# Kernel tuning notes

Measured on AMD Instinct MI355X. Metric: run time of the kernel, lower is better.

The kernel has to match this reference:

```python
import jax, jax.numpy as jnp
import numpy as np

B, T, E, A, S, H = 1024, 64, 1024, 10, 30, 200  # batch, time, embed, actdim, stoch, deter==hidden
MIN_STD = 0.1


def _xavier(key, fan_in, fan_out):
    lim = float(np.sqrt(6.0 / (fan_in + fan_out)))
    return jax.random.uniform(key, (fan_in, fan_out), jnp.float32, -lim, lim)


def setup_inputs() -> dict:
    key = jax.random.key(0)
    ks = jax.random.split(key, 20)
    gl = 1.0 / float(np.sqrt(H))  # torch GRUCell default init bound
    inp = {
        'embed': jax.random.normal(ks[0], (B, T, E), jnp.float32),
        'action': jax.random.normal(ks[1], (B, T, A), jnp.float32),
        'eps_post': jax.random.normal(ks[2], (T, B, S), jnp.float32),
        'eps_prior': jax.random.normal(ks[3], (T, B, S), jnp.float32),
        # Linear weights stored [in, out] (transposed vs torch) so x @ W works.
        'img1_w': _xavier(ks[4], A + S, H), 'img1_b': jnp.zeros((H,), jnp.float32),
        'gru_wi': jax.random.uniform(ks[5], (H, 3 * H), jnp.float32, -gl, gl),
        'gru_wh': jax.random.uniform(ks[6], (H, 3 * H), jnp.float32, -gl, gl),
        'gru_bi': jax.random.uniform(ks[7], (3 * H,), jnp.float32, -gl, gl),
        'gru_bh': jax.random.uniform(ks[8], (3 * H,), jnp.float32, -gl, gl),
        'img2_w': _xavier(ks[9], H, H), 'img2_b': jnp.zeros((H,), jnp.float32),
        'img3_w': _xavier(ks[10], H, 2 * S), 'img3_b': jnp.zeros((2 * S,), jnp.float32),
        'obs1_w': _xavier(ks[11], H + E, H), 'obs1_b': jnp.zeros((H,), jnp.float32),
        'obs2_w': _xavier(ks[12], H, 2 * S), 'obs2_b': jnp.zeros((2 * S,), jnp.float32),
    }
    return inp


def _observe(embed, action, eps_post, eps_prior,
             img1_w, img1_b, gru_wi, gru_wh, gru_bi, gru_bh,
             img2_w, img2_b, img3_w, img3_b, obs1_w, obs1_b, obs2_w, obs2_b):
    elu = jax.nn.elu
    embed_t = jnp.transpose(embed, (1, 0, 2))   # [T,B,E]
    action_t = jnp.transpose(action, (1, 0, 2))  # [T,B,A]

    def step(carry, xs):
        stoch, deter = carry
        a, emb, ep_q, ep_p = xs
        # img_step (prior)
        x = elu(jnp.concatenate([stoch, a], -1) @ img1_w + img1_b)
        gi = x @ gru_wi + gru_bi
        gh = deter @ gru_wh + gru_bh
        ir, iz, i_n = jnp.split(gi, 3, axis=-1)
        hr, hz, h_n = jnp.split(gh, 3, axis=-1)
        r = jax.nn.sigmoid(ir + hr)
        z = jax.nn.sigmoid(iz + hz)
        n = jnp.tanh(i_n + r * h_n)
        deter = (1.0 - z) * n + z * deter
        y = elu(deter @ img2_w + img2_b) @ img3_w + img3_b
        p_mean, p_std = jnp.split(y, 2, axis=-1)
        p_std = jax.nn.softplus(p_std) + MIN_STD
        p_stoch = p_mean + p_std * ep_p  # rsample
        # obs_step (posterior)
        o = elu(jnp.concatenate([deter, emb], -1) @ obs1_w + obs1_b) @ obs2_w + obs2_b
        q_mean, q_std = jnp.split(o, 2, axis=-1)
        q_std = jax.nn.softplus(q_std) + MIN_STD
        q_stoch = q_mean + q_std * ep_q  # rsample
        out = jnp.concatenate([q_mean, q_std, q_stoch, deter,
                               p_mean, p_std, p_stoch, deter], axis=-1)
        return (q_stoch, deter), out

    init = (jnp.zeros((B, S), embed.dtype), jnp.zeros((B, H), embed.dtype))
    _, outs = jax.lax.scan(step, init, (action_t, embed_t, eps_post, eps_prior))
    # outs: [T, B, 2*(3S+H)] -> [B, T, 580]; layout: post(mean,std,stoch,deter)|prior(mean,std,stoch,deter)
    return jnp.transpose(outs, (1, 0, 2))


def reference(embed, action, eps_post, eps_prior,
              img1_w, img1_b, gru_wi, gru_wh, gru_bi, gru_bh,
              img2_w, img2_b, img3_w, img3_b, obs1_w, obs1_b, obs2_w, obs2_b):
    return _observe(embed, action, eps_post, eps_prior,
                    img1_w, img1_b, gru_wi, gru_wh, gru_bi, gru_bh,
                    img2_w, img2_b, img3_w, img3_b, obs1_w, obs1_b, obs2_w, obs2_b)
```

## Files before the change

### kernel.cpp

```cpp
#include <hip/hip_runtime.h>

#define T_ 64

typedef __attribute__((ext_vector_type(4))) float f32x4;
typedef __attribute__((ext_vector_type(8))) short s16x8;

__device__ __forceinline__ unsigned short f2bf(float f) {
  unsigned u = __float_as_uint(f);
  u = (u + 0x7FFFu + ((u >> 16) & 1u)) >> 16;
  return (unsigned short)u;
}
__device__ __forceinline__ float bf2f(unsigned short h) {
  return __uint_as_float(((unsigned)h) << 16);
}
__device__ __forceinline__ float eluf(float x) { return x > 0.f ? x : __expf(x) - 1.f; }
__device__ __forceinline__ float sigmf(float x) { return 1.f / (1.f + __expf(-x)); }
__device__ __forceinline__ float tanh_(float x) {
  float xx = fminf(fmaxf(x, -30.f), 30.f);
  float e = __expf(-2.f * xx);
  return (1.f - e) / (1.f + e);
}
__device__ __forceinline__ float softpf(float x) {
  return x > 20.f ? x : __logf(1.f + __expf(x));
}

#define OPW1   0
#define OPWI   6656
#define OPWH   126464
#define OPO1D  246272
#define OPO2   286208
#define OPI2   298496
#define OPI3   345088
#define OWIWT  359424
#define OWHWT  364416
#define OO1DWT 369408
#define OI1WT  371072
#define OO2WT  372736
#define PK_U16 373248

#define OFF_PK  26214400
#define OFF_SWZ 26960896

__device__ void pack_mat(int idx, int stride, const float* __restrict__ W,
                         int K, int N, int KT, int NT, unsigned short* __restrict__ dst) {
  int total = KT * NT * 512;
  for (int i = idx; i < total; i += stride) {
    int j = i & 7, l = (i >> 3) & 63, rem = i >> 9;
    int kt = rem % KT, nt = rem / KT;
    int n = nt * 16 + (l & 15), k = kt * 32 + (l >> 4) * 8 + j;
    float v = (k < K && n < N) ? W[(size_t)k * N + n] : 0.f;
    dst[i] = f2bf(v);
  }
}

__device__ void pack_gate(int idx, int stride, const float* __restrict__ W,
                          unsigned short* __restrict__ dst) {
  int total = 3 * 13 * 6 * 512;
  for (int i = idx; i < total; i += stride) {
    int j = i & 7, l = (i >> 3) & 63, rem = i >> 9;
    int kt = rem % 6, rem2 = rem / 6, nt = rem2 % 13, g = rem2 / 13;
    int u = nt * 16 + (l & 15);
    int k = kt * 32 + (l >> 4) * 8 + j;
    float v = (u < 200) ? W[(size_t)k * 600 + g * 200 + u] : 0.f;
    dst[i] = f2bf(v);
  }
}

__global__ void prep_weights(const float* __restrict__ w1, const float* __restrict__ wi,
                             const float* __restrict__ wh, const float* __restrict__ i2,
                             const float* __restrict__ i3, const float* __restrict__ obs1w,
                             const float* __restrict__ o2,
                             unsigned short* __restrict__ pk,
                             unsigned short* __restrict__ swz) {
  int idx = blockIdx.x * blockDim.x + threadIdx.x;
  int stride = gridDim.x * blockDim.x;
  pack_mat(idx, stride, w1, 40, 200, 1, 13, pk + OPW1);
  pack_gate(idx, stride, wi, pk + OPWI);
  pack_gate(idx, stride, wh, pk + OPWH);
  pack_mat(idx, stride, obs1w, 200, 200, 6, 13, pk + OPO1D);
  pack_mat(idx, stride, o2, 200, 60, 6, 4, pk + OPO2);
  pack_mat(idx, stride, i2, 200, 200, 7, 13, pk + OPI2);
  pack_mat(idx, stride, i3, 200, 60, 7, 4, pk + OPI3);
  for (int i = idx; i < 4992; i += stride) {
    int j = i & 7, c = (i >> 3) % 208, g = i / 1664;
    pk[OWIWT + i] = f2bf((c < 200) ? wi[(size_t)(192 + j) * 600 + g * 200 + c] : 0.f);
    pk[OWHWT + i] = f2bf((c < 200) ? wh[(size_t)(192 + j) * 600 + g * 200 + c] : 0.f);
  }
  for (int i = idx; i < 1664; i += stride) {
    int c = i >> 3, j = i & 7;
    pk[OO1DWT + i] = f2bf((c < 200) ? obs1w[(size_t)(192 + j) * 200 + c] : 0.f);
    pk[OI1WT + i]  = f2bf((c < 200) ? w1[(size_t)(32 + j) * 200 + c] : 0.f);
  }
  for (int i = idx; i < 512; i += stride) {
    int c = i >> 3, j = i & 7;
    pk[OO2WT + i] = f2bf((c < 60) ? o2[(size_t)(192 + j) * 60 + c] : 0.f);
  }
  for (int i = idx; i < 212992; i += stride) {
    int j = i & 7, l = (i >> 3) & 63, rem = i >> 9;
    int nt = rem % 13, kc = rem / 13;
    int k = kc * 32 + ((l >> 4) * 8) + j;
    int n = nt * 16 + (l & 15);
    float v = (n < 200) ? obs1w[(size_t)(200 + k) * 200 + n] : 0.0f;
    swz[i] = f2bf(v);
  }
}

__global__ __launch_bounds__(256) void emb_gemm(const float* __restrict__ embed,
                                                const float* __restrict__ obs1b,
                                                const unsigned short* __restrict__ swz,
                                                unsigned short* __restrict__ emb_pre) {
  __shared__ __align__(16) unsigned short lds_A[64][40];
  int tid = threadIdx.x;
  int lane = tid & 63, w = tid >> 6;
  int R0 = blockIdx.x * 64;
  int tt = R0 >> 10;
  int bb = R0 & 1023;

  f32x4 acc[13];
#pragma unroll
  for (int nt = 0; nt < 13; ++nt) acc[nt] = (f32x4){0.f, 0.f, 0.f, 0.f};

  int i_row = tid >> 2, cg = tid & 3;
  const float* arow = embed + ((size_t)(bb + i_row) * 64 + tt) * 1024 + cg * 8;

  for (int kc = 0; kc < 32; ++kc) {
    __syncthreads();
    {
      const float* p = arow + kc * 32;
      f32x4 a0 = *(const f32x4*)p;
      f32x4 a1 = *(const f32x4*)(p + 4);
      unsigned short* dst = &lds_A[i_row][cg * 8];
      dst[0] = f2bf(a0[0]); dst[1] = f2bf(a0[1]); dst[2] = f2bf(a0[2]); dst[3] = f2bf(a0[3]);
      dst[4] = f2bf(a1[0]); dst[5] = f2bf(a1[1]); dst[6] = f2bf(a1[2]); dst[7] = f2bf(a1[3]);
    }
    __syncthreads();
    s16x8 af = *(const s16x8*)&lds_A[w * 16 + (lane & 15)][(lane >> 4) * 8];
    const unsigned short* bp = swz + (size_t)kc * 6656 + (size_t)lane * 8;
#pragma unroll
    for (int nt = 0; nt < 13; ++nt) {
      s16x8 bfv = *(const s16x8*)(bp + nt * 512);
      acc[nt] = __builtin_amdgcn_mfma_f32_16x16x32_bf16(af, bfv, acc[nt], 0, 0, 0);
    }
  }
  int r0 = R0 + w * 16 + ((lane >> 4) << 2);
  int c0 = lane & 15;
#pragma unroll
  for (int nt = 0; nt < 13; ++nt) {
    int n = nt * 16 + c0;
    if (n < 200) {
      float bv = obs1b[n];
#pragma unroll
      for (int rr = 0; rr < 4; ++rr)
        emb_pre[(size_t)(r0 + rr) * 200 + n] = f2bf(acc[nt][rr] + bv);
    }
  }
}

#define WAITVC(n) asm volatile("s_waitcnt vmcnt(" #n ")" ::: "memory")
#define LGKM0  asm volatile("s_waitcnt lgkmcnt(0)" ::: "memory")
#define MEMCLB asm volatile("" ::: "memory")
#define BAR()  __builtin_amdgcn_s_barrier()
#define SCHED0 __builtin_amdgcn_sched_barrier(0)
#define MFMA16(A, B, C) __builtin_amdgcn_mfma_f32_16x16x32_bf16((A), (B), (C), 0, 0, 0)

typedef __attribute__((address_space(3))) unsigned int u32_lds;
typedef const __attribute__((address_space(1))) unsigned int u32_glb;

__device__ __forceinline__ void gll16(const unsigned short* g, unsigned short* l, int lane) {
  __builtin_amdgcn_global_load_lds((u32_glb*)(g + lane * 8), (u32_lds*)l, 16, 0, 0);
}

__global__ __launch_bounds__(256, 1) void scan_v6(
    const float* __restrict__ action, const float* __restrict__ eps_post,
    const float* __restrict__ img1_b, const float* __restrict__ gru_bi,
    const float* __restrict__ gru_bh, const float* __restrict__ obs2_b,
    const unsigned short* __restrict__ pk, const unsigned short* __restrict__ emb_pre,
    float* __restrict__ out) {

  __shared__ __align__(16) unsigned short ring[4][12][512];
  __shared__ __align__(16) unsigned short l_w1[13 * 512];
  __shared__ __align__(16) unsigned short l_o2[24 * 512];
  __shared__ __align__(16) unsigned short l_wiWT[3][208][8];
  __shared__ __align__(16) unsigned short l_whWT[3][208][8];
  __shared__ __align__(16) unsigned short l_o1dWT[208][8];
  __shared__ __align__(16) unsigned short l_i1WT[208][8];
  __shared__ __align__(16) unsigned short l_o2WT[64][8];
  __shared__ __align__(16) unsigned short zblk[8];
  __shared__ __align__(16) unsigned short xoA[28][16][8];
  __shared__ __align__(16) unsigned short dA[28][16][8];
  __shared__ __align__(16) unsigned short sA[8][16][8];
  __shared__ __align__(16) float s_o[60][20];
  __shared__ __align__(16) float outbuf[16][292];
  __shared__ unsigned l_toff[4][96];

  const int tid = threadIdx.x, lane = tid & 63, w = tid >> 6;
  const int arow = lane & 15, kg = lane >> 4;
  const int b0 = blockIdx.x * 16;
  const int nug = (w == 0) ? 4 : 3;
  const int SW = nug * 24;
  unsigned short* ringw = &ring[w][0][0];

  for (int i = tid; i < 28 * 16 * 8; i += 256) { (&xoA[0][0][0])[i] = 0; (&dA[0][0][0])[i] = 0; }
  for (int i = tid; i < 8 * 16 * 8; i += 256) (&sA[0][0][0])[i] = 0;
  for (int i = tid; i < 13 * 512; i += 256) l_w1[i] = pk[OPW1 + i];
  for (int i = tid; i < 24 * 512; i += 256) l_o2[i] = pk[OPO2 + i];
  for (int i = tid; i < 4992; i += 256) (&l_wiWT[0][0][0])[i] = pk[OWIWT + i];
  for (int i = tid; i < 4992; i += 256) (&l_whWT[0][0][0])[i] = pk[OWHWT + i];
  for (int i = tid; i < 1664; i += 256) (&l_o1dWT[0][0])[i] = pk[OO1DWT + i];
  for (int i = tid; i < 1664; i += 256) (&l_i1WT[0][0])[i] = pk[OI1WT + i];
  for (int i = tid; i < 512; i += 256) (&l_o2WT[0][0])[i] = pk[OO2WT + i];
  if (tid < 8) zblk[tid] = 0;
  for (int i = tid; i < 4 * 96; i += 256) {
    int ww = i / 96, tau = i % 96;
    int iu = tau / 24, r2 = tau % 24, q = r2 / 6, kt = r2 % 6;
    int ug = ww + 4 * iu;
    unsigned off;
    if (q < 3) off = OPWI + (unsigned)((q * 13 + (ug <= 12 ? ug : 12)) * 6 + kt) * 512;
    else       off = OPWH + (unsigned)((2 * 13 + (ug <= 12 ? ug : 12)) * 6 + kt) * 512;
    l_toff[ww][tau] = off;
  }

  s16x8 wB[10][6];
#pragma unroll
  for (int s = 0; s < 10; ++s) {
    const unsigned short* base;
    if (w == 0) {
      if (s < 8) { int iu = s >> 1, g = s & 1; base = pk + OPWH + (size_t)((g * 13 + 4 * iu) * 6) * 512; }
      else if (s == 8) base = pk + OPO1D + (size_t)(12 * 6) * 512;
      else base = pk + OPO1D;
    } else {
      if (s < 6) { int iu = s >> 1, g = s & 1; base = pk + OPWH + (size_t)((g * 13 + (w + 4 * iu)) * 6) * 512; }
      else base = pk + OPO1D + (size_t)(((w - 1) + 3 * (s - 6)) * 6) * 512;
    }
#pragma unroll
    for (int kt = 0; kt < 6; ++kt)
      wB[s][kt] = *(const s16x8*)(base + (size_t)kt * 512 + lane * 8);
  }

  float bsum[4][2], bi2[4], bh2[4];
#pragma unroll
  for (int iu = 0; iu < 4; ++iu) {
    int u = (w + 4 * iu) * 16 + arow;
    bool vld = (iu < nug) && (u < 200);
    int uc = vld ? u : 0;
    float m = vld ? 1.f : 0.f;
    bsum[iu][0] = m * (gru_bi[uc] + gru_bh[uc]);
    bsum[iu][1] = m * (gru_bi[200 + uc] + gru_bh[200 + uc]);
    bi2[iu] = m * gru_bi[400 + uc];
    bh2[iu] = m * gru_bh[400 + uc];
  }
  float b1v[4];
#pragma unroll
  for (int i = 0; i < 4; ++i) {
    int nt = (i < 3) ? (w + 4 * i) : 12;
    int c = nt * 16 + arow;
    b1v[i] = (c < 200) ? img1_b[c] : 0.f;
  }
  float b5 = ((w * 16 + arow) < 60) ? obs2_b[w * 16 + arow] : 0.f;

  unsigned short e16[16];
#pragma unroll
  for (int i = 0; i < 4; ++i) {
    int nt4 = (w == 0) ? 12 : ((w - 1) + 3 * i);
    int c = nt4 * 16 + arow; int cc = (c < 200) ? c : 199;
#pragma unroll
    for (int rr = 0; rr < 4; ++rr)
      e16[i * 4 + rr] = emb_pre[((size_t)(b0 + kg * 4 + rr)) * 200 + cc];
  }
  float epsv[2];
  { int i1 = (tid + 256 < 480) ? tid + 256 : 479;
    epsv[0] = eps_post[((size_t)(b0 + tid / 30)) * 30 + tid % 30];
    epsv[1] = eps_post[((size_t)(b0 + i1 / 30)) * 30 + i1 % 30]; }
  float act0, actn;
  { int sl = (lane < 40) ? (w * 40 + lane) : (w * 40);
    act0 = action[((size_t)(b0 + sl / 10) * T_ + 0) * 10 + sl % 10];
    actn = action[((size_t)(b0 + sl / 10) * T_ + 1) * 10 + sl % 10]; }
  f32x4 dv[4];
#pragma unroll
  for (int iu = 0; iu < 4; ++iu) dv[iu] = (f32x4){0.f, 0.f, 0.f, 0.f};

  __syncthreads();
  if (lane < 40) {
    int sl = w * 40 + lane; int kk = sl % 10, r = sl / 10;
    sA[(30 + kk) >> 3][r][(30 + kk) & 7] = f2bf(act0);
  }
#pragma unroll
  for (int tt = 0; tt < 12; ++tt)
    gll16(pk + l_toff[w][tt], ringw + tt * 512, lane);
  WAITVC(0);
  __syncthreads();

  for (int t = 0; t < T_; ++t) {
    {
      s16x8 a0 = *(const s16x8*)&sA[kg][arow][0];
      s16x8 a1 = *(const s16x8*)&sA[4 + kg][arow][0];
#pragma unroll
      for (int i = 0; i < 4; ++i) {
        if (i < 3 || w == 0) {
          int nt = (i < 3) ? (w + 4 * i) : 12;
          int c = nt * 16 + arow;
          s16x8 B0 = *(const s16x8*)&l_w1[nt * 512 + lane * 8];
          f32x4 acc = {b1v[i], b1v[i], b1v[i], b1v[i]};
          acc = MFMA16(a0, B0, acc);
          s16x8 B1 = *(const s16x8*)((kg == 0) ? &l_i1WT[c][0] : &zblk[0]);
          acc = MFMA16(a1, B1, acc);
          if (c < 200) {
#pragma unroll
            for (int rr = 0; rr < 4; ++rr)
              xoA[c >> 3][kg * 4 + rr][c & 7] = f2bf(eluf(acc[rr]));
          }
        }
      }
    }
    LGKM0; BAR();

    {
#pragma unroll
      for (int iu = 0; iu < 4; ++iu) {
        if (iu < 3 || w == 0) {
          const int uu = (w + 4 * iu) * 16 + arow;
          const int uuc = (uu < 208) ? uu : 207;
          s16x8 ax[6], ad[6];
#pragma unroll
          for (int kt = 0; kt < 6; ++kt) {
            ax[kt] = *(const s16x8*)&xoA[kt * 4 + kg][arow][0];
            ad[kt] = *(const s16x8*)&dA[kt * 4 + kg][arow][0];
          }
          s16x8 ax6 = *(const s16x8*)&xoA[24 + kg][arow][0];
          s16x8 ad6 = *(const s16x8*)&dA[24 + kg][arow][0];
          f32x4 gv[2], gin, ghn;
#pragma unroll
          for (int q = 0; q < 4; ++q) {
            const int beta = iu * 4 + q;
            if (beta < 2) { WAITVC(30); } else { WAITVC(6); }
            float b = (q < 2) ? bsum[iu][q & 1] : ((q == 2) ? bi2[iu] : bh2[iu]);
            f32x4 acc = {b, b, b, b};
#pragma unroll
            for (int kt = 0; kt < 6; ++kt) {
              const int slot = (beta * 6 + kt) % 12;
              s16x8 Bv = *(const s16x8*)(ringw + slot * 512 + lane * 8);
              acc = MFMA16((q == 3) ? ad[kt] : ax[kt], Bv, acc);
            }
            MEMCLB; SCHED0;
#pragma unroll
            for (int k2 = 0; k2 < 6; ++k2) {
              const int ttc = beta * 6 + 12 + k2;
              int tm = (ttc >= SW) ? ttc - SW : ttc;
              gll16(pk + l_toff[w][tm], ringw + ((ttc % 12) * 512), lane);
            }
            if (q < 2) {
              { const unsigned short* wp = (kg == 0) ? &l_wiWT[q][uuc][0] : &zblk[0];
                acc = MFMA16(ax6, *(const s16x8*)wp, acc); }
              const int s_ = iu * 2 + q;
#pragma unroll
              for (int kt = 0; kt < 6; ++kt) acc = MFMA16(ad[kt], wB[s_][kt], acc);
              { const unsigned short* wp = (kg == 0) ? &l_whWT[q][uuc][0] : &zblk[0];
                acc = MFMA16(ad6, *(const s16x8*)wp, acc); }
              gv[q] = acc;
            } else if (q == 2) {
              const unsigned short* wp = (kg == 0) ? &l_wiWT[2][uuc][0] : &zblk[0];
              gin = MFMA16(ax6, *(const s16x8*)wp, acc);
            } else {
              const unsigned short* wp = (kg == 0) ? &l_whWT[2][uuc][0] : &zblk[0];
              ghn = MFMA16(ad6, *(const s16x8*)wp, acc);
            }
          }
#pragma unroll
          for (int rr = 0; rr < 4; ++rr) {
            float r = sigmf(gv[0][rr]);
            float z = sigmf(gv[1][rr]);
            float n = tanh_(gin[rr] + r * ghn[rr]);
            dv[iu][rr] = (1.f - z) * n + z * dv[iu][rr];
          }
          if (uu < 200) {
#pragma unroll
            for (int rr = 0; rr < 4; ++rr) outbuf[kg * 4 + rr][90 + uu] = dv[iu][rr];
          }
        }
      }
    }
    LGKM0; BAR();

#pragma unroll
    for (int iu = 0; iu < 4; ++iu) {
      if (iu < 3 || w == 0) {
        int uu = (w + 4 * iu) * 16 + arow;
        if (uu < 200) {
#pragma unroll
          for (int rr = 0; rr < 4; ++rr)
            dA[uu >> 3][kg * 4 + rr][uu & 7] = f2bf(dv[iu][rr]);
        }
      }
    }
    LGKM0; BAR();

    {
      s16x8 ad4[6];
#pragma unroll
      for (int kt = 0; kt < 6; ++kt) ad4[kt] = *(const s16x8*)&dA[kt * 4 + kg][arow][0];
      s16x8 ad46 = *(const s16x8*)&dA[24 + kg][arow][0];
      if (w == 0) {
        int c = 192 + arow;
        f32x4 acc = {0.f, 0.f, 0.f, 0.f};
#pragma unroll
        for (int kt = 0; kt < 6; ++kt) acc = MFMA16(ad4[kt], wB[8][kt], acc);
        { const unsigned short* wp = (kg == 0) ? &l_o1dWT[c][0] : &zblk[0];
          acc = MFMA16(ad46, *(const s16x8*)wp, acc); }
        if (c < 200) {
#pragma unroll
          for (int rr = 0; rr < 4; ++rr)
            xoA[c >> 3][kg * 4 + rr][c & 7] = f2bf(eluf(acc[rr] + bf2f(e16[rr])));
        }
      } else {
#pragma unroll
        for (int i = 0; i < 4; ++i) {
          int c = ((w - 1) + 3 * i) * 16 + arow;
          f32x4 acc = {0.f, 0.f, 0.f, 0.f};
#pragma unroll
          for (int kt = 0; kt < 6; ++kt) acc = MFMA16(ad4[kt], wB[6 + i][kt], acc);
          { const unsigned short* wp = (kg == 0) ? &l_o1dWT[c][0] : &zblk[0];
            acc = MFMA16(ad46, *(const s16x8*)wp, acc); }
#pragma unroll
          for (int rr = 0; rr < 4; ++rr)
            xoA[c >> 3][kg * 4 + rr][c & 7] = f2bf(eluf(acc[rr] + bf2f(e16[i * 4 + rr])));
        }
      }
    }
    LGKM0; BAR();

    {
      s16x8 a5[6];
#pragma unroll
      for (int kt = 0; kt < 6; ++kt) a5[kt] = *(const s16x8*)&xoA[kt * 4 + kg][arow][0];
      s16x8 a56 = *(const s16x8*)&xoA[24 + kg][arow][0];
      int c5 = w * 16 + arow;
      f32x4 acc = {b5, b5, b5, b5};
#pragma unroll
      for (int kt = 0; kt < 6; ++kt) {
        s16x8 Bv = *(const s16x8*)&l_o2[(w * 6 + kt) * 512 + lane * 8];
        acc = MFMA16(a5[kt], Bv, acc);
      }
      { const unsigned short* wp = (kg == 0) ? &l_o2WT[c5][0] : &zblk[0];
        acc = MFMA16(a56, *(const s16x8*)wp, acc); }
      if (c5 < 60) *(f32x4*)&s_o[c5][kg * 4] = acc;
    }
    LGKM0; BAR();

    {
#pragma unroll
      for (int rep = 0; rep < 2; ++rep) {
        int it = tid + rep * 256;
        bool v = it < 480;
        int itc = v ? it : 479;
        int r = itc / 30, j = itc % 30;
        float qm = s_o[j][r];
        float qs = softpf(s_o[j + 30][r]) + 0.1f;
        float qst = qm + qs * epsv[rep];
        if (v) {
          outbuf[r][j] = qm; outbuf[r][30 + j] = qs; outbuf[r][60 + j] = qst;
          sA[j >> 3][r][j & 7] = f2bf(qst);
        }
      }
      if (lane < 40) {
        int sl = w * 40 + lane; int kk = sl % 10, r = sl / 10;
        sA[(30 + kk) >> 3][r][(30 + kk) & 7] = f2bf(actn);
      }
      int tc = (t + 1 < T_) ? t + 1 : T_ - 1;
      int ta = (t + 2 < T_) ? t + 2 : T_ - 1;
#pragma unroll
      for (int i = 0; i < 4; ++i) {
        int nt4 = (w == 0) ? 12 : ((w - 1) + 3 * i);
        int c = nt4 * 16 + arow; int cc = (c < 200) ? c : 199;
#pragma unroll
        for (int rr = 0; rr < 4; ++rr)
          e16[i * 4 + rr] = emb_pre[((size_t)tc * 1024 + b0 + kg * 4 + rr) * 200 + cc];
      }
      { int i1 = (tid + 256 < 480) ? tid + 256 : 479;
        epsv[0] = eps_post[((size_t)tc * 1024 + b0 + tid / 30) * 30 + tid % 30];
        epsv[1] = eps_post[((size_t)tc * 1024 + b0 + i1 / 30) * 30 + i1 % 30]; }
      { int sl = (lane < 40) ? (w * 40 + lane) : (w * 40);
        actn = action[((size_t)(b0 + sl / 10) * T_ + ta) * 10 + sl % 10]; }
    }
    LGKM0; BAR();

#pragma unroll
    for (int k2 = 0; k2 < 5; ++k2) {
      int idx = tid + k2 * 256; idx = (idx < 1168) ? idx : 1167;
      int row = idx / 73, ci = idx - row * 73;
      f32x4 v = *(const f32x4*)&outbuf[row][ci * 4];
      *(f32x4*)(out + ((size_t)(b0 + row) * T_ + t) * 580 + ci * 4) = v;
    }
  }
}

__global__ __launch_bounds__(256) void post_head(const float* __restrict__ eps_prior,
                                                 const float* __restrict__ img2_b,
                                                 const float* __restrict__ img3_b,
                                                 const unsigned short* __restrict__ pk,
                                                 float* __restrict__ out) {
  __shared__ __align__(16) unsigned short dAp[4][28][16][8];
  __shared__ __align__(16) unsigned short y1p[4][28][16][8];
  __shared__ __align__(16) float s_p[60][68];
  int b = blockIdx.x;
  int tid = threadIdx.x;
  int lane = tid & 63, w = tid >> 6, arow = lane & 15, kg = lane >> 4;

  for (int i = tid; i < 1536; i += 256) {
    int mt = i / 384, rem = i % 384;
    int gidx = 25 + rem / 128, r2 = (rem % 128) / 8, j = rem & 7;
    dAp[mt][gidx][r2][j] = 0;
    y1p[mt][gidx][r2][j] = 0;
  }
  for (int i = tid; i < 12800; i += 256) {
    int row = i / 200, c = i % 200;
    float v = out[((size_t)(b * 64 + row)) * 580 + 90 + c];
    dAp[row >> 4][c >> 3][row & 15][c & 7] = f2bf(v);
  }
  __syncthreads();

  s16x8 ad[7];
#pragma unroll
  for (int kt = 0; kt < 7; ++kt) ad[kt] = *(const s16x8*)&dAp[w][kt * 4 + kg][arow][0];
#pragma unroll
  for (int nt = 0; nt < 13; ++nt) {
    int col = nt * 16 + arow;
    float bv = (col < 200) ? img2_b[col] : 0.f;
    f32x4 acc = {bv, bv, bv, bv};
#pragma unroll
    for (int kt = 0; kt < 7; ++kt) {
      s16x8 Bv = *(const s16x8*)(pk + OPI2 + (size_t)((nt * 7 + kt) * 512) + lane * 8);
      acc = __builtin_amdgcn_mfma_f32_16x16x32_bf16(ad[kt], Bv, acc, 0, 0, 0);
    }
    if (col < 200) {
#pragma unroll
      for (int rr = 0; rr < 4; ++rr)
        y1p[w][col >> 3][kg * 4 + rr][col & 7] = f2bf(eluf(acc[rr]));
    }
  }
  __syncthreads();

  s16x8 ay[7];
#pragma unroll
  for (int kt = 0; kt < 7; ++kt) ay[kt] = *(const s16x8*)&y1p[w][kt * 4 + kg][arow][0];
#pragma unroll
  for (int nt = 0; nt < 4; ++nt) {
    int col = nt * 16 + arow;
    float bv = (col < 60) ? img3_b[col] : 0.f;
    f32x4 acc = {bv, bv, bv, bv};
#pragma unroll
    for (int kt = 0; kt < 7; ++kt) {
      s16x8 Bv = *(const s16x8*)(pk + OPI3 + (size_t)((nt * 7 + kt) * 512) + lane * 8);
      acc = __builtin_amdgcn_mfma_f32_16x16x32_bf16(ay[kt], Bv, acc, 0, 0, 0);
    }
    if (col < 60) {
#pragma unroll
      for (int rr = 0; rr < 4; ++rr) s_p[col][w * 16 + kg * 4 + rr] = acc[rr];
    }
  }
  __syncthreads();

  for (int i = tid; i < 1920; i += 256) {
    int row = i / 30, j = i % 30;
    float pm = s_p[j][row];
    float ps = softpf(s_p[j + 30][row]) + 0.1f;
    float pst = pm + ps * eps_prior[((size_t)row * 1024 + b) * 30 + j];
    size_t ob = ((size_t)b * 64 + row) * 580;
    out[ob + 290 + j] = pm;
    out[ob + 320 + j] = ps;
    out[ob + 350 + j] = pst;
  }
  for (int i = tid; i < 6400; i += 256) {
    int row = i / 100, c2 = i % 100;
    size_t ob = ((size_t)b * 64 + row) * 580;
    *(float2*)&out[ob + 380 + c2 * 2] = *(const float2*)&out[ob + 90 + c2 * 2];
  }
}

extern "C" void kernel_launch(void* const* d_in, const int* in_sizes, int n_in,
                              void* d_out, int out_size, void* d_ws, size_t ws_size,
                              hipStream_t stream) {
  const float* embed    = (const float*)d_in[0];
  const float* action   = (const float*)d_in[1];
  const float* eps_post = (const float*)d_in[2];
  const float* eps_prior= (const float*)d_in[3];
  const float* img1_w   = (const float*)d_in[4];
  const float* img1_b   = (const float*)d_in[5];
  const float* gru_wi   = (const float*)d_in[6];
  const float* gru_wh   = (const float*)d_in[7];
  const float* gru_bi   = (const float*)d_in[8];
  const float* gru_bh   = (const float*)d_in[9];
  const float* img2_w   = (const float*)d_in[10];
  const float* img2_b   = (const float*)d_in[11];
  const float* img3_w   = (const float*)d_in[12];
  const float* img3_b   = (const float*)d_in[13];
  const float* obs1_w   = (const float*)d_in[14];
  const float* obs1_b   = (const float*)d_in[15];
  const float* obs2_w   = (const float*)d_in[16];
  const float* obs2_b   = (const float*)d_in[17];

  char* ws = (char*)d_ws;
  unsigned short* emb_pre = (unsigned short*)ws;
  unsigned short* pkw     = (unsigned short*)(ws + OFF_PK);
  unsigned short* swz     = (unsigned short*)(ws + OFF_SWZ);
  float* outp = (float*)d_out;

  prep_weights<<<256, 256, 0, stream>>>(img1_w, gru_wi, gru_wh, img2_w, img3_w,
                                        obs1_w, obs2_w, pkw, swz);
  emb_gemm<<<1024, 256, 0, stream>>>(embed, obs1_b, swz, emb_pre);
  scan_v6<<<64, 256, 0, stream>>>(action, eps_post, img1_b, gru_bi, gru_bh,
                                  obs2_b, pkw, emb_pre, outp);
  post_head<<<1024, 256, 0, stream>>>(eps_prior, img2_b, img3_b, pkw, outp);
}
```

Baseline: 996.2 us.

## Double scan block to 8 waves and redistribute GRU/obs tiles with streamed weight ring

```diff
diff --git a/kernel.cpp b/kernel.cpp
--- a/kernel.cpp
+++ b/kernel.cpp
@@ -156,12 +156,14 @@
   }
 }
 
-#define WAITVC(n) asm volatile("s_waitcnt vmcnt(" #n ")" ::: "memory")
 #define LGKM0  asm volatile("s_waitcnt lgkmcnt(0)" ::: "memory")
 #define MEMCLB asm volatile("" ::: "memory")
 #define BAR()  __builtin_amdgcn_s_barrier()
-#define SCHED0 __builtin_amdgcn_sched_barrier(0)
 #define MFMA16(A, B, C) __builtin_amdgcn_mfma_f32_16x16x32_bf16((A), (B), (C), 0, 0, 0)
+#define WV9  asm volatile("s_waitcnt vmcnt(9)" ::: "memory")
+#define WV29 asm volatile("s_waitcnt vmcnt(29)" ::: "memory")
+#define WV4  asm volatile("s_waitcnt vmcnt(4)" ::: "memory")
+#define WV0  asm volatile("s_waitcnt vmcnt(0)" ::: "memory")
 
 typedef __attribute__((address_space(3))) unsigned int u32_lds;
 typedef const __attribute__((address_space(1))) unsigned int u32_glb;
@@ -170,16 +172,62 @@
   __builtin_amdgcn_global_load_lds((u32_glb*)(g + lane * 8), (u32_lds*)l, 16, 0, 0);
 }
 
-__global__ __launch_bounds__(256, 1) void scan_v6(
+template <int TB, bool BIGB>
+__device__ __forceinline__ f32x4 cons6(const s16x8* A, f32x4 acc,
+                                       unsigned short* ringw, const unsigned* toffw,
+                                       const unsigned short* pk, int lane) {
+#pragma unroll
+  for (int kt = 0; kt < 6; ++kt) {
+    const int tau = TB + kt;
+    if ((tau & 3) == 0) {
+      if (tau < 8) { if (BIGB) { WV29; } else { WV9; } }
+      else { WV4; }
+    }
+    s16x8 Bv = *(const s16x8*)(ringw + (tau & 7) * 512 + lane * 8);
+    acc = MFMA16(A[kt], Bv, acc);
+    if ((tau & 3) == 3) {
+      LGKM0; MEMCLB;
+#pragma unroll
+      for (int k2 = 1; k2 <= 4; ++k2) {
+        const int tile = (tau + 4 + k2) % 48;
+        gll16(pk + toffw[tile], ringw + (tile & 7) * 512, lane);
+      }
+      MEMCLB;
+    }
+  }
+  return acc;
+}
+
+__device__ __forceinline__ f32x4 res6(const s16x8* A, const s16x8* Wt, f32x4 acc) {
+#pragma unroll
+  for (int kt = 0; kt < 6; ++kt) acc = MFMA16(A[kt], Wt[kt], acc);
+  return acc;
+}
+__device__ __forceinline__ f32x4 rem1(const s16x8& A6, const unsigned short* wt,
+                                      const unsigned short* zb, bool kg0, f32x4 acc) {
+  const unsigned short* p = kg0 ? wt : zb;
+  return MFMA16(A6, *(const s16x8*)p, acc);
+}
+__device__ __forceinline__ void grustep(const f32x4& rv, const f32x4& zv,
+                                        const f32x4& inv, const f32x4& hnv, f32x4& dv) {
+#pragma unroll
+  for (int rr = 0; rr < 4; ++rr) {
+    float r = sigmf(rv[rr]);
+    float z = sigmf(zv[rr]);
+    float n = tanh_(inv[rr] + r * hnv[rr]);
+    dv[rr] = (1.f - z) * n + z * dv[rr];
+  }
+}
+
+__global__ __launch_bounds__(512, 1) void scan_v7(
     const float* __restrict__ action, const float* __restrict__ eps_post,
     const float* __restrict__ img1_b, const float* __restrict__ gru_bi,
     const float* __restrict__ gru_bh, const float* __restrict__ obs2_b,
     const unsigned short* __restrict__ pk, const unsigned short* __restrict__ emb_pre,
     float* __restrict__ out) {
 
-  __shared__ __align__(16) unsigned short ring[4][12][512];
+  __shared__ __align__(16) unsigned short ring[8][8][512];
   __shared__ __align__(16) unsigned short l_w1[13 * 512];
-  __shared__ __align__(16) unsigned short l_o2[24 * 512];
   __shared__ __align__(16) unsigned short l_wiWT[3][208][8];
   __shared__ __align__(16) unsigned short l_whWT[3][208][8];
   __shared__ __align__(16) unsigned short l_o1dWT[208][8];
@@ -191,305 +239,345 @@
   __shared__ __align__(16) unsigned short sA[8][16][8];
   __shared__ __align__(16) float s_o[60][20];
   __shared__ __align__(16) float outbuf[16][292];
-  __shared__ unsigned l_toff[4][96];
+  __shared__ unsigned l_toff[8][48];
 
   const int tid = threadIdx.x, lane = tid & 63, w = tid >> 6;
   const int arow = lane & 15, kg = lane >> 4;
+  const bool kg0 = (kg == 0);
   const int b0 = blockIdx.x * 16;
-  const int nug = (w == 0) ? 4 : 3;
-  const int SW = nug * 24;
   unsigned short* ringw = &ring[w][0][0];
-
-  for (int i = tid; i < 28 * 16 * 8; i += 256) { (&xoA[0][0][0])[i] = 0; (&dA[0][0][0])[i] = 0; }
-  for (int i = tid; i < 8 * 16 * 8; i += 256) (&sA[0][0][0])[i] = 0;
-  for (int i = tid; i < 13 * 512; i += 256) l_w1[i] = pk[OPW1 + i];
-  for (int i = tid; i < 24 * 512; i += 256) l_o2[i] = pk[OPO2 + i];
-  for (int i = tid; i < 4992; i += 256) (&l_wiWT[0][0][0])[i] = pk[OWIWT + i];
-  for (int i = tid; i < 4992; i += 256) (&l_whWT[0][0][0])[i] = pk[OWHWT + i];
-  for (int i = tid; i < 1664; i += 256) (&l_o1dWT[0][0])[i] = pk[OO1DWT + i];
-  for (int i = tid; i < 1664; i += 256) (&l_i1WT[0][0])[i] = pk[OI1WT + i];
-  for (int i = tid; i < 512; i += 256) (&l_o2WT[0][0])[i] = pk[OO2WT + i];
+  const unsigned* toffw = &l_toff[w][0];
+
+  for (int i = tid; i < 28 * 16 * 8; i += 512) { (&xoA[0][0][0])[i] = 0; (&dA[0][0][0])[i] = 0; }
+  for (int i = tid; i < 8 * 16 * 8; i += 512) (&sA[0][0][0])[i] = 0;
+  for (int i = tid; i < 13 * 512; i += 512) l_w1[i] = pk[OPW1 + i];
+  for (int i = tid; i < 4992; i += 512) {
+    (&l_wiWT[0][0][0])[i] = pk[OWIWT + i];
+    (&l_whWT[0][0][0])[i] = pk[OWHWT + i];
+  }
+  for (int i = tid; i < 1664; i += 512) {
+    (&l_o1dWT[0][0])[i] = pk[OO1DWT + i];
+    (&l_i1WT[0][0])[i] = pk[OI1WT + i];
+  }
+  for (int i = tid; i < 512; i += 512) (&l_o2WT[0][0])[i] = pk[OO2WT + i];
   if (tid < 8) zblk[tid] = 0;
-  for (int i = tid; i < 4 * 96; i += 256) {
-    int ww = i / 96, tau = i % 96;
-    int iu = tau / 24, r2 = tau % 24, q = r2 / 6, kt = r2 % 6;
-    int ug = ww + 4 * iu;
+  for (int i = tid; i < 8 * 48; i += 512) {
+    int ww = i / 48, tau = i % 48;
     unsigned off;
-    if (q < 3) off = OPWI + (unsigned)((q * 13 + (ug <= 12 ? ug : 12)) * 6 + kt) * 512;
-    else       off = OPWH + (unsigned)((2 * 13 + (ug <= 12 ? ug : 12)) * 6 + kt) * 512;
+    if (ww < 5) {
+      if (tau < 18) { int g = tau / 6, kt = tau % 6; off = OPWI + ((g * 13 + ww) * 6 + kt) * 512; }
+      else {
+        int t2 = tau - 18, ug = ww + 8;
+        if (t2 < 6)       off = OPWI + ((0 * 13 + ug) * 6 + t2) * 512;
+        else if (t2 < 12) off = OPWI + ((1 * 13 + ug) * 6 + (t2 - 6)) * 512;
+        else if (t2 < 18) off = OPWH + ((1 * 13 + ug) * 6 + (t2 - 12)) * 512;
+        else if (t2 < 24) off = OPWI + ((2 * 13 + ug) * 6 + (t2 - 18)) * 512;
+        else              off = OPWH + ((2 * 13 + ug) * 6 + (t2 - 24)) * 512;
+      }
+    } else {
+      if (tau < 18) { int g = tau / 6, kt = tau % 6; off = OPWI + ((g * 13 + ww) * 6 + kt) * 512; }
+      else if (tau < 42) {
+        int i4 = (tau - 18) / 6, kt = (tau - 18) % 6;
+        int nt = (ww - 5) * 4 + i4;
+        off = OPO1D + (nt * 6 + kt) * 512;
+      } else {
+        int kt = tau - 42;
+        int nt5 = (ww == 5) ? 0 : (ww == 6) ? 1 : 3;
+        off = OPO2 + (nt5 * 6 + kt) * 512;
+      }
+    }
     l_toff[ww][tau] = off;
   }
 
-  s16x8 wB[10][6];
-#pragma unroll
-  for (int s = 0; s < 10; ++s) {
-    const unsigned short* base;
-    if (w == 0) {
-      if (s < 8) { int iu = s >> 1, g = s & 1; base = pk + OPWH + (size_t)((g * 13 + 4 * iu) * 6) * 512; }
-      else if (s == 8) base = pk + OPO1D + (size_t)(12 * 6) * 512;
-      else base = pk + OPO1D;
+  s16x8 wB[4][6];
+  {
+    const unsigned short* base[4];
+    if (w < 5) {
+      base[0] = pk + OPWH + (size_t)((0 * 13 + w) * 6) * 512;
+      base[1] = pk + OPWH + (size_t)((1 * 13 + w) * 6) * 512;
+      base[2] = pk + OPWH + (size_t)((2 * 13 + w) * 6) * 512;
+      base[3] = pk + OPWH + (size_t)((0 * 13 + w + 8) * 6) * 512;
     } else {
-      if (s < 6) { int iu = s >> 1, g = s & 1; base = pk + OPWH + (size_t)((g * 13 + (w + 4 * iu)) * 6) * 512; }
-      else base = pk + OPO1D + (size_t)(((w - 1) + 3 * (s - 6)) * 6) * 512;
-    }
-#pragma unroll
-    for (int kt = 0; kt < 6; ++kt)
-      wB[s][kt] = *(const s16x8*)(base + (size_t)kt * 512 + lane * 8);
-  }
-
-  float bsum[4][2], bi2[4], bh2[4];
-#pragma unroll
-  for (int iu = 0; iu < 4; ++iu) {
-    int u = (w + 4 * iu) * 16 + arow;
-    bool vld = (iu < nug) && (u < 200);
-    int uc = vld ? u : 0;
-    float m = vld ? 1.f : 0.f;
-    bsum[iu][0] = m * (gru_bi[uc] + gru_bh[uc]);
-    bsum[iu][1] = m * (gru_bi[200 + uc] + gru_bh[200 + uc]);
-    bi2[iu] = m * gru_bi[400 + uc];
-    bh2[iu] = m * gru_bh[400 + uc];
-  }
-  float b1v[4];
-#pragma unroll
-  for (int i = 0; i < 4; ++i) {
-    int nt = (i < 3) ? (w + 4 * i) : 12;
-    int c = nt * 16 + arow;
-    b1v[i] = (c < 200) ? img1_b[c] : 0.f;
-  }
-  float b5 = ((w * 16 + arow) < 60) ? obs2_b[w * 16 + arow] : 0.f;
-
-  unsigned short e16[16];
-#pragma unroll
-  for (int i = 0; i < 4; ++i) {
-    int nt4 = (w == 0) ? 12 : ((w - 1) + 3 * i);
-    int c = nt4 * 16 + arow; int cc = (c < 200) ? c : 199;
-#pragma unroll
-    for (int rr = 0; rr < 4; ++rr)
-      e16[i * 4 + rr] = emb_pre[((size_t)(b0 + kg * 4 + rr)) * 200 + cc];
-  }
-  float epsv[2];
-  { int i1 = (tid + 256 < 480) ? tid + 256 : 479;
-    epsv[0] = eps_post[((size_t)(b0 + tid / 30)) * 30 + tid % 30];
-    epsv[1] = eps_post[((size_t)(b0 + i1 / 30)) * 30 + i1 % 30]; }
+      base[0] = pk + OPWH + (size_t)((0 * 13 + w) * 6) * 512;
+      base[1] = pk + OPWH + (size_t)((1 * 13 + w) * 6) * 512;
+      base[2] = pk + OPWH + (size_t)((2 * 13 + w) * 6) * 512;
+      if (w == 5)      base[3] = pk + OPO1D + (size_t)(12 * 6) * 512;
+      else if (w == 7) base[3] = pk + OPO2 + (size_t)(2 * 6) * 512;
+      else             base[3] = pk + OPO1D;
+    }
+#pragma unroll
+    for (int s = 0; s < 4; ++s)
+#pragma unroll
+      for (int kt = 0; kt < 6; ++kt)
+        wB[s][kt] = *(const s16x8*)(base[s] + (size_t)kt * 512 + lane * 8);
+  }
+
+  const int uA = w * 16 + arow;
+  const int uB = (w + 8) * 16 + arow;
+  const bool mB = (w < 5) && (uB < 200);
+  const int uBc = (uB < 200) ? uB : 199;
+  float bsA0 = gru_bi[uA] + gru_bh[uA];
+  float bsA1 = gru_bi[200 + uA] + gru_bh[200 + uA];
+  float bi2a = gru_bi[400 + uA], bh2a = gru_bh[400 + uA];
+  float bsB0 = mB ? (gru_bi[uBc] + gru_bh[uBc]) : 0.f;
+  float bsB1 = mB ? (gru_bi[200 + uBc] + gru_bh[200 + uBc]) : 0.f;
+  float bi2b = mB ? gru_bi[400 + uBc] : 0.f;
+  float bh2b = mB ? gru_bh[400 + uBc] : 0.f;
+  float b1A = img1_b[uA];
+  float b1B = mB ? img1_b[uBc] : 0.f;
+  float b5a = 0.f, b5b = 0.f;
+  if (w == 5) b5a = obs2_b[arow];
+  else if (w == 6) b5a = obs2_b[16 + arow];
+  else if (w == 7) { b5a = (48 + arow < 60) ? obs2_b[48 + arow] : 0.f; b5b = obs2_b[32 + arow]; }
+
+  unsigned short e16[20];
+#pragma unroll
+  for (int i = 0; i < 20; ++i) e16[i] = 0;
+  if (w >= 5) {
+#pragma unroll
+    for (int i = 0; i < 5; ++i) {
+      int nt = (w == 5) ? ((i < 4) ? i : 12) : ((w == 6) ? (4 + ((i < 4) ? i : 3)) : (8 + ((i < 4) ? i : 3)));
+      int c = nt * 16 + arow; int cc = (c < 200) ? c : 199;
+#pragma unroll
+      for (int rr = 0; rr < 4; ++rr)
+        e16[i * 4 + rr] = emb_pre[((size_t)(b0 + kg * 4 + rr)) * 200 + cc];
+    }
+  }
+  float epsv;
+  { int it = (tid < 480) ? tid : 479;
+    epsv = eps_post[((size_t)(b0 + it / 30)) * 30 + it % 30]; }
   float act0, actn;
-  { int sl = (lane < 40) ? (w * 40 + lane) : (w * 40);
+  { int sl = (lane < 20) ? (w * 20 + lane) : (w * 20);
     act0 = action[((size_t)(b0 + sl / 10) * T_ + 0) * 10 + sl % 10];
     actn = action[((size_t)(b0 + sl / 10) * T_ + 1) * 10 + sl % 10]; }
-  f32x4 dv[4];
-#pragma unroll
-  for (int iu = 0; iu < 4; ++iu) dv[iu] = (f32x4){0.f, 0.f, 0.f, 0.f};
+  f32x4 dv0 = {0.f, 0.f, 0.f, 0.f}, dv1 = {0.f, 0.f, 0.f, 0.f};
 
   __syncthreads();
-  if (lane < 40) {
-    int sl = w * 40 + lane; int kk = sl % 10, r = sl / 10;
+  if (lane < 20) {
+    int sl = w * 20 + lane; int kk = sl % 10, r = sl / 10;
     sA[(30 + kk) >> 3][r][(30 + kk) & 7] = f2bf(act0);
   }
 #pragma unroll
-  for (int tt = 0; tt < 12; ++tt)
-    gll16(pk + l_toff[w][tt], ringw + tt * 512, lane);
-  WAITVC(0);
+  for (int tt = 0; tt < 8; ++tt) gll16(pk + toffw[tt], ringw + tt * 512, lane);
+  WV0;
   __syncthreads();
 
   for (int t = 0; t < T_; ++t) {
     {
       s16x8 a0 = *(const s16x8*)&sA[kg][arow][0];
       s16x8 a1 = *(const s16x8*)&sA[4 + kg][arow][0];
-#pragma unroll
-      for (int i = 0; i < 4; ++i) {
-        if (i < 3 || w == 0) {
-          int nt = (i < 3) ? (w + 4 * i) : 12;
-          int c = nt * 16 + arow;
-          s16x8 B0 = *(const s16x8*)&l_w1[nt * 512 + lane * 8];
-          f32x4 acc = {b1v[i], b1v[i], b1v[i], b1v[i]};
-          acc = MFMA16(a0, B0, acc);
-          s16x8 B1 = *(const s16x8*)((kg == 0) ? &l_i1WT[c][0] : &zblk[0]);
-          acc = MFMA16(a1, B1, acc);
-          if (c < 200) {
-#pragma unroll
-            for (int rr = 0; rr < 4; ++rr)
-              xoA[c >> 3][kg * 4 + rr][c & 7] = f2bf(eluf(acc[rr]));
-          }
+      {
+        s16x8 B0 = *(const s16x8*)&l_w1[w * 512 + lane * 8];
+        f32x4 acc = {b1A, b1A, b1A, b1A};
+        acc = MFMA16(a0, B0, acc);
+        acc = rem1(a1, &l_i1WT[uA][0], zblk, kg0, acc);
+#pragma unroll
+        for (int rr = 0; rr < 4; ++rr)
+          xoA[uA >> 3][kg * 4 + rr][uA & 7] = f2bf(eluf(acc[rr]));
+      }
+      if (w < 5) {
+        s16x8 B0 = *(const s16x8*)&l_w1[(w + 8) * 512 + lane * 8];
+        f32x4 acc = {b1B, b1B, b1B, b1B};
+        acc = MFMA16(a0, B0, acc);
+        acc = rem1(a1, &l_i1WT[uB][0], zblk, kg0, acc);
+        if (uB < 200) {
+#pragma unroll
+          for (int rr = 0; rr < 4; ++rr)
+            xoA[uB >> 3][kg * 4 + rr][uB & 7] = f2bf(eluf(acc[rr]));
         }
       }
     }
     LGKM0; BAR();
 
     {
-#pragma unroll
-      for (int iu = 0; iu < 4; ++iu) {
-        if (iu < 3 || w == 0) {
-          const int uu = (w + 4 * iu) * 16 + arow;
-          const int uuc = (uu < 208) ? uu : 207;
-          s16x8 ax[6], ad[6];
-#pragma unroll
-          for (int kt = 0; kt < 6; ++kt) {
-            ax[kt] = *(const s16x8*)&xoA[kt * 4 + kg][arow][0];
-            ad[kt] = *(const s16x8*)&dA[kt * 4 + kg][arow][0];
-          }
-          s16x8 ax6 = *(const s16x8*)&xoA[24 + kg][arow][0];
-          s16x8 ad6 = *(const s16x8*)&dA[24 + kg][arow][0];
-          f32x4 gv[2], gin, ghn;
-#pragma unroll
-          for (int q = 0; q < 4; ++q) {
-            const int beta = iu * 4 + q;
-            if (beta < 2) { WAITVC(30); } else { WAITVC(6); }
-            float b = (q < 2) ? bsum[iu][q & 1] : ((q == 2) ? bi2[iu] : bh2[iu]);
-            f32x4 acc = {b, b, b, b};
-#pragma unroll
-            for (int kt = 0; kt < 6; ++kt) {
-              const int slot = (beta * 6 + kt) % 12;
-              s16x8 Bv = *(const s16x8*)(ringw + slot * 512 + lane * 8);
-              acc = MFMA16((q == 3) ? ad[kt] : ax[kt], Bv, acc);
-            }
-            MEMCLB; SCHED0;
-#pragma unroll
-            for (int k2 = 0; k2 < 6; ++k2) {
-              const int ttc = beta * 6 + 12 + k2;
-              int tm = (ttc >= SW) ? ttc - SW : ttc;
-              gll16(pk + l_toff[w][tm], ringw + ((ttc % 12) * 512), lane);
-            }
-            if (q < 2) {
-              { const unsigned short* wp = (kg == 0) ? &l_wiWT[q][uuc][0] : &zblk[0];
-                acc = MFMA16(ax6, *(const s16x8*)wp, acc); }
-              const int s_ = iu * 2 + q;
-#pragma unroll
-              for (int kt = 0; kt < 6; ++kt) acc = MFMA16(ad[kt], wB[s_][kt], acc);
-              { const unsigned short* wp = (kg == 0) ? &l_whWT[q][uuc][0] : &zblk[0];
-                acc = MFMA16(ad6, *(const s16x8*)wp, acc); }
-              gv[q] = acc;
-            } else if (q == 2) {
-              const unsigned short* wp = (kg == 0) ? &l_wiWT[2][uuc][0] : &zblk[0];
-              gin = MFMA16(ax6, *(const s16x8*)wp, acc);
-            } else {
-              const unsigned short* wp = (kg == 0) ? &l_whWT[2][uuc][0] : &zblk[0];
-              ghn = MFMA16(ad6, *(const s16x8*)wp, acc);
-            }
-          }
-#pragma unroll
-          for (int rr = 0; rr < 4; ++rr) {
-            float r = sigmf(gv[0][rr]);
-            float z = sigmf(gv[1][rr]);
-            float n = tanh_(gin[rr] + r * ghn[rr]);
-            dv[iu][rr] = (1.f - z) * n + z * dv[iu][rr];
-          }
-          if (uu < 200) {
-#pragma unroll
-            for (int rr = 0; rr < 4; ++rr) outbuf[kg * 4 + rr][90 + uu] = dv[iu][rr];
-          }
+      s16x8 ax[6], ad[6];
+#pragma unroll
+      for (int kt = 0; kt < 6; ++kt) {
+        ax[kt] = *(const s16x8*)&xoA[kt * 4 + kg][arow][0];
+        ad[kt] = *(const s16x8*)&dA[kt * 4 + kg][arow][0];
+      }
+      s16x8 ax6 = *(const s16x8*)&xoA[24 + kg][arow][0];
+      s16x8 ad6 = *(const s16x8*)&dA[24 + kg][arow][0];
+      if (w < 5) {
+        f32x4 rv = cons6<0, false>(ax, (f32x4){bsA0, bsA0, bsA0, bsA0}, ringw, toffw, pk, lane);
+        rv = rem1(ax6, &l_wiWT[0][uA][0], zblk, kg0, rv);
+        rv = res6(ad, wB[0], rv);
+        rv = rem1(ad6, &l_whWT[0][uA][0], zblk, kg0, rv);
+        f32x4 zv = cons6<6, false>(ax, (f32x4){bsA1, bsA1, bsA1, bsA1}, ringw, toffw, pk, lane);
+        zv = rem1(ax6, &l_wiWT[1][uA][0], zblk, kg0, zv);
+        zv = res6(ad, wB[1], zv);
+        zv = rem1(ad6, &l_whWT[1][uA][0], zblk, kg0, zv);
+        f32x4 inv = cons6<12, false>(ax, (f32x4){bi2a, bi2a, bi2a, bi2a}, ringw, toffw, pk, lane);
+        inv = rem1(ax6, &l_wiWT[2][uA][0], zblk, kg0, inv);
+        f32x4 hnv = res6(ad, wB[2], (f32x4){bh2a, bh2a, bh2a, bh2a});
+        hnv = rem1(ad6, &l_whWT[2][uA][0], zblk, kg0, hnv);
+        grustep(rv, zv, inv, hnv, dv0);
+#pragma unroll
+        for (int rr = 0; rr < 4; ++rr) outbuf[kg * 4 + rr][90 + uA] = dv0[rr];
+        f32x4 rv2 = cons6<18, false>(ax, (f32x4){bsB0, bsB0, bsB0, bsB0}, ringw, toffw, pk, lane);
+        rv2 = rem1(ax6, &l_wiWT[0][uB][0], zblk, kg0, rv2);
+        rv2 = res6(ad, wB[3], rv2);
+        rv2 = rem1(ad6, &l_whWT[0][uB][0], zblk, kg0, rv2);
+        f32x4 zv2 = cons6<24, false>(ax, (f32x4){bsB1, bsB1, bsB1, bsB1}, ringw, toffw, pk, lane);
+        zv2 = cons6<30, false>(ad, zv2, ringw, toffw, pk, lane);
+        zv2 = rem1(ax6, &l_wiWT[1][uB][0], zblk, kg0, zv2);
+        zv2 = rem1(ad6, &l_whWT[1][uB][0], zblk, kg0, zv2);
+        f32x4 inv2 = cons6<36, false>(ax, (f32x4){bi2b, bi2b, bi2b, bi2b}, ringw, toffw, pk, lane);
+        inv2 = rem1(ax6, &l_wiWT[2][uB][0], zblk, kg0, inv2);
+        f32x4 hnv2 = cons6<42, false>(ad, (f32x4){bh2b, bh2b, bh2b, bh2b}, ringw, toffw, pk, lane);
+        hnv2 = rem1(ad6, &l_whWT[2][uB][0], zblk, kg0, hnv2);
+        grustep(rv2, zv2, inv2, hnv2, dv1);
+        if (uB < 200) {
+#pragma unroll
+          for (int rr = 0; rr < 4; ++rr) outbuf[kg * 4 + rr][90 + uB] = dv1[rr];
         }
+      } else {
+        f32x4 rv = cons6<0, true>(ax, (f32x4){bsA0, bsA0, bsA0, bsA0}, ringw, toffw, pk, lane);
+        rv = rem1(ax6, &l_wiWT[0][uA][0], zblk, kg0, rv);
+        rv = res6(ad, wB[0], rv);
+        rv = rem1(ad6, &l_whWT[0][uA][0], zblk, kg0, rv);
+        f32x4 zv = cons6<6, true>(ax, (f32x4){bsA1, bsA1, bsA1, bsA1}, ringw, toffw, pk, lane);
+        zv = rem1(ax6, &l_wiWT[1][uA][0], zblk, kg0, zv);
+        zv = res6(ad, wB[1], zv);
+        zv = rem1(ad6, &l_whWT[1][uA][0], zblk, kg0, zv);
+        f32x4 inv = cons6<12, true>(ax, (f32x4){bi2a, bi2a, bi2a, bi2a}, ringw, toffw, pk, lane);
+        inv = rem1(ax6, &l_wiWT[2][uA][0], zblk, kg0, inv);
+        f32x4 hnv = res6(ad, wB[2], (f32x4){bh2a, bh2a, bh2a, bh2a});
+        hnv = rem1(ad6, &l_whWT[2][uA][0], zblk, kg0, hnv);
+        grustep(rv, zv, inv, hnv, dv0);
+#pragma unroll
+        for (int rr = 0; rr < 4; ++rr) outbuf[kg * 4 + rr][90 + uA] = dv0[rr];
       }
     }
     LGKM0; BAR();
 
-#pragma unroll
-    for (int iu = 0; iu < 4; ++iu) {
-      if (iu < 3 || w == 0) {
-        int uu = (w + 4 * iu) * 16 + arow;
-        if (uu < 200) {
-#pragma unroll
-          for (int rr = 0; rr < 4; ++rr)
-            dA[uu >> 3][kg * 4 + rr][uu & 7] = f2bf(dv[iu][rr]);
-        }
+    {
+#pragma unroll
+      for (int rr = 0; rr < 4; ++rr)
+        dA[uA >> 3][kg * 4 + rr][uA & 7] = f2bf(dv0[rr]);
+      if (mB) {
+#pragma unroll
+        for (int rr = 0; rr < 4; ++rr)
+          dA[uB >> 3][kg * 4 + rr][uB & 7] = f2bf(dv1[rr]);
       }
     }
     LGKM0; BAR();
 
-    {
+    if (w >= 5) {
       s16x8 ad4[6];
 #pragma unroll
       for (int kt = 0; kt < 6; ++kt) ad4[kt] = *(const s16x8*)&dA[kt * 4 + kg][arow][0];
       s16x8 ad46 = *(const s16x8*)&dA[24 + kg][arow][0];
-      if (w == 0) {
+      const int ntb = (w - 5) * 4;
+      {
+        int c = (ntb + 0) * 16 + arow;
+        f32x4 acc = cons6<18, true>(ad4, (f32x4){0.f, 0.f, 0.f, 0.f}, ringw, toffw, pk, lane);
+        acc = rem1(ad46, &l_o1dWT[c][0], zblk, kg0, acc);
+#pragma unroll
+        for (int rr = 0; rr < 4; ++rr)
+          xoA[c >> 3][kg * 4 + rr][c & 7] = f2bf(eluf(acc[rr] + bf2f(e16[0 * 4 + rr])));
+      }
+      {
+        int c = (ntb + 1) * 16 + arow;
+        f32x4 acc = cons6<24, true>(ad4, (f32x4){0.f, 0.f, 0.f, 0.f}, ringw, toffw, pk, lane);
+        acc = rem1(ad46, &l_o1dWT[c][0], zblk, kg0, acc);
+#pragma unroll
+        for (int rr = 0; rr < 4; ++rr)
+          xoA[c >> 3][kg * 4 + rr][c & 7] = f2bf(eluf(acc[rr] + bf2f(e16[1 * 4 + rr])));
+      }
+      {
+        int c = (ntb + 2) * 16 + arow;
+        f32x4 acc = cons6<30, true>(ad4, (f32x4){0.f, 0.f, 0.f, 0.f}, ringw, toffw, pk, lane);
+        acc = rem1(ad46, &l_o1dWT[c][0], zblk, kg0, acc);
+#pragma unroll
+        for (int rr = 0; rr < 4; ++rr)
+          xoA[c >> 3][kg * 4 + rr][c & 7] = f2bf(eluf(acc[rr] + bf2f(e16[2 * 4 + rr])));
+      }
+      {
+        int c = (ntb + 3) * 16 + arow;
+        f32x4 acc = cons6<36, true>(ad4, (f32x4){0.f, 0.f, 0.f, 0.f}, ringw, toffw, pk, lane);
+        acc = rem1(ad46, &l_o1dWT[c][0], zblk, kg0, acc);
+#pragma unroll
+        for (int rr = 0; rr < 4; ++rr)
+          xoA[c >> 3][kg * 4 + rr][c & 7] = f2bf(eluf(acc[rr] + bf2f(e16[3 * 4 + rr])));
+      }
+      if (w == 5) {
         int c = 192 + arow;
-        f32x4 acc = {0.f, 0.f, 0.f, 0.f};
-#pragma unroll
-        for (int kt = 0; kt < 6; ++kt) acc = MFMA16(ad4[kt], wB[8][kt], acc);
-        { const unsigned short* wp = (kg == 0) ? &l_o1dWT[c][0] : &zblk[0];
-          acc = MFMA16(ad46, *(const s16x8*)wp, acc); }
+        f32x4 acc = res6(ad4, wB[3], (f32x4){0.f, 0.f, 0.f, 0.f});
+        acc = rem1(ad46, &l_o1dWT[c][0], zblk, kg0, acc);
         if (c < 200) {
 #pragma unroll
           for (int rr = 0; rr < 4; ++rr)
-            xoA[c >> 3][kg * 4 + rr][c & 7] = f2bf(eluf(acc[rr] + bf2f(e16[rr])));
+            xoA[c >> 3][kg * 4 + rr][c & 7] = f2bf(eluf(acc[rr] + bf2f(e16[16 + rr])));
         }
-      } else {
-#pragma unroll
-        for (int i = 0; i < 4; ++i) {
-          int c = ((w - 1) + 3 * i) * 16 + arow;
-          f32x4 acc = {0.f, 0.f, 0.f, 0.f};
-#pragma unroll
-          for (int kt = 0; kt < 6; ++kt) acc = MFMA16(ad4[kt], wB[6 + i][kt], acc);
-          { const unsigned short* wp = (kg == 0) ? &l_o1dWT[c][0] : &zblk[0];
-            acc = MFMA16(ad46, *(const s16x8*)wp, acc); }
-#pragma unroll
-          for (int rr = 0; rr < 4; ++rr)
-            xoA[c >> 3][kg * 4 + rr][c & 7] = f2bf(eluf(acc[rr] + bf2f(e16[i * 4 + rr])));
-        }
       }
     }
     LGKM0; BAR();
 
-    {
+    if (w >= 5) {
       s16x8 a5[6];
 #pragma unroll
       for (int kt = 0; kt < 6; ++kt) a5[kt] = *(const s16x8*)&xoA[kt * 4 + kg][arow][0];
       s16x8 a56 = *(const s16x8*)&xoA[24 + kg][arow][0];
-      int c5 = w * 16 + arow;
-      f32x4 acc = {b5, b5, b5, b5};
-#pragma unroll
-      for (int kt = 0; kt < 6; ++kt) {
-        s16x8 Bv = *(const s16x8*)&l_o2[(w * 6 + kt) * 512 + lane * 8];
-        acc = MFMA16(a5[kt], Bv, acc);
-      }
-      { const unsigned short* wp = (kg == 0) ? &l_o2WT[c5][0] : &zblk[0];
-        acc = MFMA16(a56, *(const s16x8*)wp, acc); }
+      int c5 = (w == 5) ? arow : (w == 6) ? (16 + arow) : (48 + arow);
+      f32x4 acc = cons6<42, true>(a5, (f32x4){b5a, b5a, b5a, b5a}, ringw, toffw, pk, lane);
+      {
+        int c5c = (c5 < 64) ? c5 : 63;
+        acc = rem1(a56, &l_o2WT[c5c][0], zblk, kg0, acc);
+      }
       if (c5 < 60) *(f32x4*)&s_o[c5][kg * 4] = acc;
+      if (w == 7) {
+        int c5r = 32 + arow;
+        f32x4 acc2 = res6(a5, wB[3], (f32x4){b5b, b5b, b5b, b5b});
+        acc2 = rem1(a56, &l_o2WT[c5r][0], zblk, kg0, acc2);
+        *(f32x4*)&s_o[c5r][kg * 4] = acc2;
+      }
     }
     LGKM0; BAR();
 
+    MEMCLB;
     {
-#pragma unroll
-      for (int rep = 0; rep < 2; ++rep) {
-        int it = tid + rep * 256;
-        bool v = it < 480;
-        int itc = v ? it : 479;
-        int r = itc / 30, j = itc % 30;
+      if (tid < 480) {
+        int r = tid / 30, j = tid % 30;
         float qm = s_o[j][r];
         float qs = softpf(s_o[j + 30][r]) + 0.1f;
-        float qst = qm + qs * epsv[rep];
-        if (v) {
-          outbuf[r][j] = qm; outbuf[r][30 + j] = qs; outbuf[r][60 + j] = qst;
-          sA[j >> 3][r][j & 7] = f2bf(qst);
-        }
-      }
-      if (lane < 40) {
-        int sl = w * 40 + lane; int kk = sl % 10, r = sl / 10;
+        float qst = qm + qs * epsv;
+        outbuf[r][j] = qm; outbuf[r][30 + j] = qs; outbuf[r][60 + j] = qst;
+        sA[j >> 3][r][j & 7] = f2bf(qst);
+      }
+      if (lane < 20) {
+        int sl = w * 20 + lane; int kk = sl % 10, r = sl / 10;
         sA[(30 + kk) >> 3][r][(30 + kk) & 7] = f2bf(actn);
       }
       int tc = (t + 1 < T_) ? t + 1 : T_ - 1;
       int ta = (t + 2 < T_) ? t + 2 : T_ - 1;
-#pragma unroll
-      for (int i = 0; i < 4; ++i) {
-        int nt4 = (w == 0) ? 12 : ((w - 1) + 3 * i);
-        int c = nt4 * 16 + arow; int cc = (c < 200) ? c : 199;
-#pragma unroll
-        for (int rr = 0; rr < 4; ++rr)
-          e16[i * 4 + rr] = emb_pre[((size_t)tc * 1024 + b0 + kg * 4 + rr) * 200 + cc];
-      }
-      { int i1 = (tid + 256 < 480) ? tid + 256 : 479;
-        epsv[0] = eps_post[((size_t)tc * 1024 + b0 + tid / 30) * 30 + tid % 30];
-        epsv[1] = eps_post[((size_t)tc * 1024 + b0 + i1 / 30) * 30 + i1 % 30]; }
-      { int sl = (lane < 40) ? (w * 40 + lane) : (w * 40);
+      MEMCLB;
+      if (w >= 5) {
+#pragma unroll
+        for (int i = 0; i < 5; ++i) {
+          int nt = (w == 5) ? ((i < 4) ? i : 12) : ((w == 6) ? (4 + ((i < 4) ? i : 3)) : (8 + ((i < 4) ? i : 3)));
+          int c = nt * 16 + arow; int cc = (c < 200) ? c : 199;
+#pragma unroll
+          for (int rr = 0; rr < 4; ++rr)
+            e16[i * 4 + rr] = emb_pre[((size_t)tc * 1024 + b0 + kg * 4 + rr) * 200 + cc];
+        }
+      }
+      { int it = (tid < 480) ? tid : 479;
+        epsv = eps_post[((size_t)tc * 1024 + b0 + it / 30) * 30 + it % 30]; }
+      { int sl = (lane < 20) ? (w * 20 + lane) : (w * 20);
         actn = action[((size_t)(b0 + sl / 10) * T_ + ta) * 10 + sl % 10]; }
+      MEMCLB;
     }
     LGKM0; BAR();
 
 #pragma unroll
-    for (int k2 = 0; k2 < 5; ++k2) {
-      int idx = tid + k2 * 256; idx = (idx < 1168) ? idx : 1167;
+    for (int k2 = 0; k2 < 3; ++k2) {
+      int idx = tid + k2 * 512; idx = (idx < 1168) ? idx : 1167;
       int row = idx / 73, ci = idx - row * 73;
       f32x4 v = *(const f32x4*)&outbuf[row][ci * 4];
       *(f32x4*)(out + ((size_t)(b0 + row) * T_ + t) * 580 + ci * 4) = v;
     }
+    MEMCLB;
   }
 }
 
@@ -607,7 +695,7 @@
   prep_weights<<<256, 256, 0, stream>>>(img1_w, gru_wi, gru_wh, img2_w, img3_w,
                                         obs1_w, obs2_w, pkw, swz);
   emb_gemm<<<1024, 256, 0, stream>>>(embed, obs1_b, swz, emb_pre);
-  scan_v6<<<64, 256, 0, stream>>>(action, eps_post, img1_b, gru_bi, gru_bh,
+  scan_v7<<<64, 512, 0, stream>>>(action, eps_post, img1_b, gru_bi, gru_bh,
                                   obs2_b, pkw, emb_pre, outp);
   post_head<<<1024, 256, 0, stream>>>(eps_prior, img2_b, img3_b, pkw, outp);
 }
```

Result: slower. 1.067 ms (+7.1%).
